# Kernel optimization log

Hardware: AMD Instinct MI355X
Metric: run time of the kernel (lower is better)

## Reference

```python
import jax, jax.numpy as jnp
import numpy as np

N = 12000       # num nodes
E = 384000      # num edges (avg degree 32)
F_IN = 512      # num_feats
H = 64          # gnn_hid_dim (== anchor_dim)
C = 7           # num_cls
SIGMA = 1.0


def setup_inputs() -> dict:
    key = jax.random.key(0)
    ks = jax.random.split(key, 9)
    scale = lambda fan_in: 1.0 / np.sqrt(fan_in)
    return {
        "x": jax.random.normal(ks[0], (N, F_IN), dtype=jnp.float32),
        "W1": jax.random.normal(ks[1], (F_IN, H), dtype=jnp.float32) * scale(F_IN),
        "b1": jnp.zeros((H,), dtype=jnp.float32),
        "W2": jax.random.normal(ks[2], (H, H), dtype=jnp.float32) * scale(H),
        "b2": jnp.zeros((H,), dtype=jnp.float32),
        "aux": jax.random.normal(ks[3], (H,), dtype=jnp.float32),
        "clf_W": jax.random.normal(ks[4], (2 * H, C), dtype=jnp.float32) * scale(2 * H),
        "clf_b": jnp.zeros((C,), dtype=jnp.float32),
        "edge_index": jax.random.randint(ks[5], (2, E), 0, N, dtype=jnp.int64),
    }


def gcn_conv(x, W, b, src, dst, n):
    # GCNConv: D^{-1/2} (A + I) D^{-1/2} X W + b, with self-loops
    h = x @ W                                                   # [N, out]
    deg = jax.ops.segment_sum(jnp.ones(src.shape[0], h.dtype), dst,
                              num_segments=n) + 1.0             # +1 for self-loop
    inv_sqrt = jax.lax.rsqrt(deg)
    norm = inv_sqrt[src] * inv_sqrt[dst]                        # [E]
    agg = jax.ops.segment_sum(h[src] * norm[:, None], dst, num_segments=n)
    agg = agg + h / deg[:, None]                                # self-loop term (norm = 1/deg)
    return agg + b


def reference(x, W1, b1, W2, b2, aux, clf_W, clf_b, edge_index):
    src, dst = edge_index[0], edge_index[1]
    n = x.shape[0]
    h = jax.nn.relu(gcn_conv(x, W1, b1, src, dst, n))
    h = gcn_conv(h, W2, b2, src, dst, n)                        # [N, H]
    # kernel aggregate: pairwise Gaussian kernel on cosine scores
    a = aux / jnp.maximum(jnp.linalg.norm(aux), 1e-12)          # F.normalize
    hn = jnp.maximum(jnp.linalg.norm(h, axis=-1), 1e-8)         # cosine_similarity eps
    score = (h @ a) / hn                                        # [N]
    diff = score[None, :] - score[:, None]                      # [N, N]
    kappa = jnp.exp(-(diff * diff) / (SIGMA * SIGMA))           # [N, N]
    z = (kappa @ h) / jnp.sum(kappa, axis=1, keepdims=True)     # [N, H]
    return jnp.concatenate([h, z], axis=-1) @ clf_W + clf_b     # [N, C]
```

## Files before the change

### kernel.cpp

```cpp
#include <hip/hip_runtime.h>
#include <hip/hip_bf16.h>

#define N_NODES 12000
#define N_EDGES 384000
#define F_IN 512
#define H 64
#define C_CLS 7
#define KTERMS 16
#define PAD 96
#define CSTR 32
#define MOM_BLKS 768
#define MSTR 1040
#define NB 4
#define GEMM_BLKS 375
#define FILL_BLKS 256
#define XS_STR 68

__device__ __forceinline__ float wred_f(float x) {
    #pragma unroll
    for (int o = 32; o > 0; o >>= 1) x += __shfl_xor(x, o);
    return x;
}

__global__ __launch_bounds__(256) void init_k(int* __restrict__ cur,
                                              double* __restrict__ M8) {
    int i = blockIdx.x * 256 + threadIdx.x;
    if (i < N_NODES) cur[i * CSTR] = 0;
    if (i < 8 * MSTR) M8[i] = 0.0;
}

__global__ __launch_bounds__(256) void k1_gemm_fill(const float* __restrict__ x,
                                                    const float* __restrict__ W1,
                                                    const int* __restrict__ ei,
                                                    float* __restrict__ hbuf,
                                                    int* __restrict__ cur,
                                                    int* __restrict__ csrc) {
    const int b = blockIdx.x, t = threadIdx.x;
    if (b < GEMM_BLKS) {
        __shared__ float xs[32 * XS_STR];
        __shared__ float wsm[64 * 64];
        const int tx = t & 15, ty = t >> 4;
        const int i0 = b * 32;
        float acc[2][4] = {};
        for (int k0 = 0; k0 < F_IN; k0 += 64) {
            #pragma unroll
            for (int q = 0; q < 2; ++q) {
                int idx = t + q * 256;
                int row = idx >> 4, kg = idx & 15;
                *(float4*)(&xs[row * XS_STR + kg * 4]) =
                    *(const float4*)(x + (size_t)(i0 + row) * F_IN + k0 + kg * 4);
            }
            #pragma unroll
            for (int q = 0; q < 4; ++q) {
                int idx = t + q * 256;
                int r = idx >> 4, cg = idx & 15;
                *(float4*)(&wsm[r * 64 + cg * 4]) =
                    *(const float4*)(W1 + (size_t)(k0 + r) * H + cg * 4);
            }
            __syncthreads();
            #pragma unroll
            for (int kk0 = 0; kk0 < 64; kk0 += 4) {
                float4 a0 = *(const float4*)(&xs[(ty * 2 + 0) * XS_STR + kk0]);
                float4 a1 = *(const float4*)(&xs[(ty * 2 + 1) * XS_STR + kk0]);
                float4 b0 = *(const float4*)(&wsm[(kk0 + 0) * 64 + tx * 4]);
                float4 b1v = *(const float4*)(&wsm[(kk0 + 1) * 64 + tx * 4]);
                float4 b2v = *(const float4*)(&wsm[(kk0 + 2) * 64 + tx * 4]);
                float4 b3v = *(const float4*)(&wsm[(kk0 + 3) * 64 + tx * 4]);
                acc[0][0] += a0.x * b0.x;  acc[0][1] += a0.x * b0.y;  acc[0][2] += a0.x * b0.z;  acc[0][3] += a0.x * b0.w;
                acc[0][0] += a0.y * b1v.x; acc[0][1] += a0.y * b1v.y; acc[0][2] += a0.y * b1v.z; acc[0][3] += a0.y * b1v.w;
                acc[0][0] += a0.z * b2v.x; acc[0][1] += a0.z * b2v.y; acc[0][2] += a0.z * b2v.z; acc[0][3] += a0.z * b2v.w;
                acc[0][0] += a0.w * b3v.x; acc[0][1] += a0.w * b3v.y; acc[0][2] += a0.w * b3v.z; acc[0][3] += a0.w * b3v.w;
                acc[1][0] += a1.x * b0.x;  acc[1][1] += a1.x * b0.y;  acc[1][2] += a1.x * b0.z;  acc[1][3] += a1.x * b0.w;
                acc[1][0] += a1.y * b1v.x; acc[1][1] += a1.y * b1v.y; acc[1][2] += a1.y * b1v.z; acc[1][3] += a1.y * b1v.w;
                acc[1][0] += a1.z * b2v.x; acc[1][1] += a1.z * b2v.y; acc[1][2] += a1.z * b2v.z; acc[1][3] += a1.z * b2v.w;
                acc[1][0] += a1.w * b3v.x; acc[1][1] += a1.w * b3v.y; acc[1][2] += a1.w * b3v.z; acc[1][3] += a1.w * b3v.w;
            }
            __syncthreads();
        }
        #pragma unroll
        for (int r = 0; r < 2; ++r) {
            int row = i0 + ty * 2 + r;
            *(float4*)(hbuf + (size_t)row * H + tx * 4) =
                make_float4(acc[r][0], acc[r][1], acc[r][2], acc[r][3]);
        }
    } else {
        for (int e = (b - GEMM_BLKS) * 256 + t; e < N_EDGES; e += FILL_BLKS * 256) {
            int s = ei[e];
            int d = ei[N_EDGES + e];
            int pos = atomicAdd(&cur[d * CSTR], 1);
            if (pos < PAD) csrc[d * PAD + pos] = s;
        }
    }
}

__global__ __launch_bounds__(256) void agg1_k(const float* __restrict__ hbuf,
                                              const float* __restrict__ b1,
                                              const int* __restrict__ cur,
                                              const int* __restrict__ csrc,
                                              float* __restrict__ h1) {
    __shared__ int2 sPair[NB * PAD];
    __shared__ int sDeg[NB];
    __shared__ float sIsd[NB];
    const int t = threadIdx.x, f = t & 63, w = t >> 6;
    const int base = blockIdx.x * NB;
    if (t < NB) {
        int d = cur[(base + t) * CSTR];
        sDeg[t] = min(d, PAD);
        sIsd[t] = rsqrtf((float)d + 1.f);
    }
    __syncthreads();
    for (int idx = t; idx < NB * PAD; idx += 256) {
        int n = idx / PAD, e = idx - n * PAD;
        if (e < sDeg[n]) {
            int s = csrc[(base + n) * PAD + e];
            sPair[idx] = make_int2(s, __float_as_int(rsqrtf((float)cur[s * CSTR] + 1.f)));
        }
    }
    __syncthreads();
    const int i = base + w;
    const int deg = sDeg[w];
    const float isd = sIsd[w];
    const int2* pp = sPair + w * PAD;
    float acc = 0.f;
    int e = 0;
    for (; e + 8 <= deg; e += 8) {
        int2 p0 = pp[e], p1 = pp[e+1], p2 = pp[e+2], p3 = pp[e+3];
        int2 p4 = pp[e+4], p5 = pp[e+5], p6 = pp[e+6], p7 = pp[e+7];
        acc += hbuf[p0.x * H + f] * __int_as_float(p0.y)
             + hbuf[p1.x * H + f] * __int_as_float(p1.y)
             + hbuf[p2.x * H + f] * __int_as_float(p2.y)
             + hbuf[p3.x * H + f] * __int_as_float(p3.y)
             + hbuf[p4.x * H + f] * __int_as_float(p4.y)
             + hbuf[p5.x * H + f] * __int_as_float(p5.y)
             + hbuf[p6.x * H + f] * __int_as_float(p6.y)
             + hbuf[p7.x * H + f] * __int_as_float(p7.y);
    }
    for (; e + 4 <= deg; e += 4) {
        int2 p0 = pp[e], p1 = pp[e+1], p2 = pp[e+2], p3 = pp[e+3];
        acc += hbuf[p0.x * H + f] * __int_as_float(p0.y)
             + hbuf[p1.x * H + f] * __int_as_float(p1.y)
             + hbuf[p2.x * H + f] * __int_as_float(p2.y)
             + hbuf[p3.x * H + f] * __int_as_float(p3.y);
    }
    for (; e < deg; ++e) {
        int2 p = pp[e];
        acc += hbuf[p.x * H + f] * __int_as_float(p.y);
    }
    float res = (acc + hbuf[i * H + f] * isd) * isd + b1[f];
    h1[i * H + f] = fmaxf(res, 0.f);
}

__global__ __launch_bounds__(256) void agg2_k(const float* __restrict__ h1,
                                              const float* __restrict__ W2,
                                              const float* __restrict__ b2,
                                              const float* __restrict__ aux,
                                              const int* __restrict__ cur,
                                              const int* __restrict__ csrc,
                                              float* __restrict__ h2,
                                              float* __restrict__ score) {
    __shared__ float w2s[64 * 64];
    __shared__ int2 sPair[NB * PAD];
    __shared__ int sDeg[NB];
    __shared__ float sIsd[NB];
    __shared__ float anorm[64];
    __shared__ float gsh[NB * 64];
    const int t = threadIdx.x, f = t & 63, w = t >> 6;
    const int base = blockIdx.x * NB;
    #pragma unroll
    for (int q = 0; q < 4; ++q) {
        int idx = t + q * 256;
        int r = idx >> 4, c4 = idx & 15;
        *(float4*)(&w2s[r * 64 + c4 * 4]) = *(const float4*)(W2 + r * H + c4 * 4);
    }
    if (t < NB) {
        int d = cur[(base + t) * CSTR];
        sDeg[t] = min(d, PAD);
        sIsd[t] = rsqrtf((float)d + 1.f);
    }
    if (t < 64) {
        float av = aux[t];
        anorm[t] = av * rsqrtf(fmaxf(wred_f(av * av), 1e-24f));
    }
    __syncthreads();
    for (int idx = t; idx < NB * PAD; idx += 256) {
        int n = idx / PAD, e = idx - n * PAD;
        if (e < sDeg[n]) {
            int s = csrc[(base + n) * PAD + e];
            sPair[idx] = make_int2(s, __float_as_int(rsqrtf((float)cur[s * CSTR] + 1.f)));
        }
    }
    __syncthreads();
    const int i = base + w;
    const int deg = sDeg[w];
    const float isd = sIsd[w];
    const int2* pp = sPair + w * PAD;
    float acc = 0.f;
    int e = 0;
    for (; e + 8 <= deg; e += 8) {
        int2 p0 = pp[e], p1 = pp[e+1], p2 = pp[e+2], p3 = pp[e+3];
        int2 p4 = pp[e+4], p5 = pp[e+5], p6 = pp[e+6], p7 = pp[e+7];
        acc += h1[p0.x * H + f] * __int_as_float(p0.y)
             + h1[p1.x * H + f] * __int_as_float(p1.y)
             + h1[p2.x * H + f] * __int_as_float(p2.y)
             + h1[p3.x * H + f] * __int_as_float(p3.y)
             + h1[p4.x * H + f] * __int_as_float(p4.y)
             + h1[p5.x * H + f] * __int_as_float(p5.y)
             + h1[p6.x * H + f] * __int_as_float(p6.y)
             + h1[p7.x * H + f] * __int_as_float(p7.y);
    }
    for (; e + 4 <= deg; e += 4) {
        int2 p0 = pp[e], p1 = pp[e+1], p2 = pp[e+2], p3 = pp[e+3];
        acc += h1[p0.x * H + f] * __int_as_float(p0.y)
             + h1[p1.x * H + f] * __int_as_float(p1.y)
             + h1[p2.x * H + f] * __int_as_float(p2.y)
             + h1[p3.x * H + f] * __int_as_float(p3.y);
    }
    for (; e < deg; ++e) {
        int2 p = pp[e];
        acc += h1[p.x * H + f] * __int_as_float(p.y);
    }
    float g = (acc + h1[i * H + f] * isd) * isd;
    gsh[w * 64 + f] = g;
    __builtin_amdgcn_wave_barrier();
    float hv = b2[f];
    #pragma unroll 16
    for (int k = 0; k < 64; ++k) hv += gsh[w * 64 + k] * w2s[k * 64 + f];
    h2[i * H + f] = hv;
    float dp = wred_f(hv * anorm[f]);
    float nn = wred_f(hv * hv);
    if (f == 0) score[i] = dp / fmaxf(sqrtf(nn), 1e-8f);
}

__global__ __launch_bounds__(256) void momden_k(const float* __restrict__ h2,
                                                const float* __restrict__ score,
                                                double* __restrict__ M8) {
    const int t = threadIdx.x, f = t & 63, g = t >> 6;
    float accM[KTERMS], accD[KTERMS];
    #pragma unroll
    for (int k = 0; k < KTERMS; ++k) { accM[k] = 0.f; accD[k] = 0.f; }
    for (int j = blockIdx.x * 4 + g; j < N_NODES; j += MOM_BLKS * 4) {
        float sj = score[j];
        float wj = expf(-sj * sj);
        float hv = h2[j * H + f];
        float tm = wj * hv, td = wj;
        #pragma unroll
        for (int k = 0; k < KTERMS; ++k) {
            accM[k] += tm; tm *= sj;
            accD[k] += td; td *= sj;
        }
    }
    __shared__ float Msh[4 * KTERMS * 64];
    __shared__ float Dsh[4 * KTERMS];
    #pragma unroll
    for (int k = 0; k < KTERMS; ++k) Msh[(g * KTERMS + k) * 64 + f] = accM[k];
    if (f == 0) {
        #pragma unroll
        for (int k = 0; k < KTERMS; ++k) Dsh[g * KTERMS + k] = accD[k];
    }
    __syncthreads();
    double* Mc = M8 + (size_t)(blockIdx.x & 7) * MSTR;
    for (int idx = t; idx < KTERMS * 64; idx += 256) {
        int k = idx >> 6, ff = idx & 63;
        float sum = Msh[(0 * KTERMS + k) * 64 + ff] + Msh[(1 * KTERMS + k) * 64 + ff]
                  + Msh[(2 * KTERMS + k) * 64 + ff] + Msh[(3 * KTERMS + k) * 64 + ff];
        unsafeAtomicAdd(&Mc[idx], (double)sum);
    }
    if (t < KTERMS) {
        float sum = Dsh[t] + Dsh[KTERMS + t] + Dsh[2 * KTERMS + t] + Dsh[3 * KTERMS + t];
        unsafeAtomicAdd(&Mc[1024 + t], (double)sum);
    }
}

__global__ __launch_bounds__(256) void final_k(const float* __restrict__ h2,
                                               const float* __restrict__ score,
                                               const double* __restrict__ M8,
                                               const float* __restrict__ clfW,
                                               const float* __restrict__ clfb,
                                               float* __restrict__ out) {
    __shared__ float Ms[KTERMS * 64];
    __shared__ float m0s[KTERMS];
    __shared__ float cw[128 * C_CLS];
    __shared__ float cb[8];
    __shared__ float zh[4 * 128];
    const int t = threadIdx.x, f = t & 63, w = t >> 6;
    for (int idx = t; idx < KTERMS * 64; idx += 256) {
        double s = 0.0;
        #pragma unroll
        for (int c = 0; c < 8; ++c) s += M8[(size_t)c * MSTR + idx];
        Ms[idx] = (float)s;
    }
    if (t < KTERMS) {
        double s = 0.0;
        #pragma unroll
        for (int c = 0; c < 8; ++c) s += M8[(size_t)c * MSTR + 1024 + t];
        m0s[t] = (float)s;
    }
    for (int idx = t; idx < 128 * C_CLS; idx += 256) cw[idx] = clfW[idx];
    if (t < C_CLS) cb[t] = clfb[t];
    __syncthreads();
    const int base = blockIdx.x * 16;
    for (int q = 0; q < 4; ++q) {
        int i = base + q * 4 + w;
        float s = score[i];
        float c = expf(-s * s);
        float t2 = 2.f * s;
        float num = 0.f, den = 0.f;
        #pragma unroll
        for (int k = 0; k < KTERMS; ++k) {
            num += c * Ms[k * 64 + f];
            den += c * m0s[k];
            c *= t2 * (1.0f / (float)(k + 1));
        }
        zh[w * 128 + f] = h2[i * H + f];
        zh[w * 128 + 64 + f] = num / den;
        __builtin_amdgcn_wave_barrier();
        if (f < C_CLS) {
            float o = cb[f];
            #pragma unroll 8
            for (int u = 0; u < 128; ++u) o += zh[w * 128 + u] * cw[u * C_CLS + f];
            out[(size_t)i * C_CLS + f] = o;
        }
        __builtin_amdgcn_wave_barrier();
    }
}

extern "C" void kernel_launch(void* const* d_in, const int* in_sizes, int n_in,
                              void* d_out, int out_size, void* d_ws, size_t ws_size,
                              hipStream_t stream) {
    (void)in_sizes; (void)n_in; (void)out_size; (void)ws_size;
    const float* x    = (const float*)d_in[0];
    const float* W1   = (const float*)d_in[1];
    const float* b1   = (const float*)d_in[2];
    const float* W2   = (const float*)d_in[3];
    const float* b2   = (const float*)d_in[4];
    const float* aux  = (const float*)d_in[5];
    const float* clfW = (const float*)d_in[6];
    const float* clfb = (const float*)d_in[7];
    const int*   ei   = (const int*)d_in[8];
    float* out = (float*)d_out;
    char* ws = (char*)d_ws;

    float*  hbuf  = (float*)(ws + 0);
    float*  h1    = (float*)(ws + 3072000);
    float*  h2    = (float*)(ws + 6144000);
    float*  score = (float*)(ws + 9216000);
    int*    csrc  = (int*)  (ws + 9264000);
    int*    cur   = (int*)  (ws + 13872000);
    double* M8    = (double*)(ws + 15408000);

    init_k<<<47, 256, 0, stream>>>(cur, M8);
    k1_gemm_fill<<<GEMM_BLKS + FILL_BLKS, 256, 0, stream>>>(x, W1, ei, hbuf, cur, csrc);
    agg1_k<<<N_NODES / NB, 256, 0, stream>>>(hbuf, b1, cur, csrc, h1);
    agg2_k<<<N_NODES / NB, 256, 0, stream>>>(h1, W2, b2, aux, cur, csrc, h2, score);
    momden_k<<<MOM_BLKS, 256, 0, stream>>>(h2, score, M8);
    final_k<<<750, 256, 0, stream>>>(h2, score, M8, clfW, clfb, out);
}
```

Measured before the change: 95.13 us.

## Split-K the first GEMM with 64-row tiles and atomic accumulation

The X@W1 GEMM now uses 64-row tiles with a 4x4 per-thread register block, and the K dimension is split in two halves across block pairs. The partial results are combined with float atomic adds into hbuf, which init_k now zeroes. The goal is more register reuse per shared-memory load while keeping about the same block count for parallelism. In exchange it adds a zeroing pass over hbuf, atomic traffic, and non-deterministic summation order.

```diff
diff --git a/kernel.cpp b/kernel.cpp
--- a/kernel.cpp
+++ b/kernel.cpp
@@ -12,7 +12,7 @@
 #define MOM_BLKS 768
 #define MSTR 1040
 #define NB 4
-#define GEMM_BLKS 375
+#define GEMM_BLKS 376
 #define FILL_BLKS 256
 #define XS_STR 68
 
@@ -22,11 +22,14 @@
     return x;
 }
 
-__global__ __launch_bounds__(256) void init_k(int* __restrict__ cur,
+__global__ __launch_bounds__(256) void init_k(float* __restrict__ hbuf,
+                                              int* __restrict__ cur,
                                               double* __restrict__ M8) {
-    int i = blockIdx.x * 256 + threadIdx.x;
-    if (i < N_NODES) cur[i * CSTR] = 0;
-    if (i < 8 * MSTR) M8[i] = 0.0;
+    const int tid = blockIdx.x * 256 + threadIdx.x;
+    const float4 z4 = make_float4(0.f, 0.f, 0.f, 0.f);
+    for (int i = tid; i < N_NODES * H / 4; i += 48128) ((float4*)hbuf)[i] = z4;
+    if (tid < N_NODES) cur[tid * CSTR] = 0;
+    if (tid < 8 * MSTR) M8[tid] = 0.0;
 }
 
 __global__ __launch_bounds__(256) void k1_gemm_fill(const float* __restrict__ x,
@@ -37,18 +40,20 @@
                                                     int* __restrict__ csrc) {
     const int b = blockIdx.x, t = threadIdx.x;
     if (b < GEMM_BLKS) {
-        __shared__ float xs[32 * XS_STR];
+        __shared__ float xs[64 * XS_STR];
         __shared__ float wsm[64 * 64];
         const int tx = t & 15, ty = t >> 4;
-        const int i0 = b * 32;
-        float acc[2][4] = {};
-        for (int k0 = 0; k0 < F_IN; k0 += 64) {
+        const int ks = b & 1;
+        const int i0 = (b >> 1) * 64;
+        float acc[4][4] = {};
+        for (int k0 = ks * 256; k0 < ks * 256 + 256; k0 += 64) {
             #pragma unroll
-            for (int q = 0; q < 2; ++q) {
+            for (int q = 0; q < 4; ++q) {
                 int idx = t + q * 256;
                 int row = idx >> 4, kg = idx & 15;
+                int rg = min(i0 + row, N_NODES - 1);
                 *(float4*)(&xs[row * XS_STR + kg * 4]) =
-                    *(const float4*)(x + (size_t)(i0 + row) * F_IN + k0 + kg * 4);
+                    *(const float4*)(x + (size_t)rg * F_IN + k0 + kg * 4);
             }
             #pragma unroll
             for (int q = 0; q < 4; ++q) {
@@ -60,8 +65,10 @@
             __syncthreads();
             #pragma unroll
             for (int kk0 = 0; kk0 < 64; kk0 += 4) {
-                float4 a0 = *(const float4*)(&xs[(ty * 2 + 0) * XS_STR + kk0]);
-                float4 a1 = *(const float4*)(&xs[(ty * 2 + 1) * XS_STR + kk0]);
+                float4 a0 = *(const float4*)(&xs[(ty * 4 + 0) * XS_STR + kk0]);
+                float4 a1 = *(const float4*)(&xs[(ty * 4 + 1) * XS_STR + kk0]);
+                float4 a2 = *(const float4*)(&xs[(ty * 4 + 2) * XS_STR + kk0]);
+                float4 a3 = *(const float4*)(&xs[(ty * 4 + 3) * XS_STR + kk0]);
                 float4 b0 = *(const float4*)(&wsm[(kk0 + 0) * 64 + tx * 4]);
                 float4 b1v = *(const float4*)(&wsm[(kk0 + 1) * 64 + tx * 4]);
                 float4 b2v = *(const float4*)(&wsm[(kk0 + 2) * 64 + tx * 4]);
@@ -74,14 +81,25 @@
                 acc[1][0] += a1.y * b1v.x; acc[1][1] += a1.y * b1v.y; acc[1][2] += a1.y * b1v.z; acc[1][3] += a1.y * b1v.w;
                 acc[1][0] += a1.z * b2v.x; acc[1][1] += a1.z * b2v.y; acc[1][2] += a1.z * b2v.z; acc[1][3] += a1.z * b2v.w;
                 acc[1][0] += a1.w * b3v.x; acc[1][1] += a1.w * b3v.y; acc[1][2] += a1.w * b3v.z; acc[1][3] += a1.w * b3v.w;
+                acc[2][0] += a2.x * b0.x;  acc[2][1] += a2.x * b0.y;  acc[2][2] += a2.x * b0.z;  acc[2][3] += a2.x * b0.w;
+                acc[2][0] += a2.y * b1v.x; acc[2][1] += a2.y * b1v.y; acc[2][2] += a2.y * b1v.z; acc[2][3] += a2.y * b1v.w;
+                acc[2][0] += a2.z * b2v.x; acc[2][1] += a2.z * b2v.y; acc[2][2] += a2.z * b2v.z; acc[2][3] += a2.z * b2v.w;
+                acc[2][0] += a2.w * b3v.x; acc[2][1] += a2.w * b3v.y; acc[2][2] += a2.w * b3v.z; acc[2][3] += a2.w * b3v.w;
+                acc[3][0] += a3.x * b0.x;  acc[3][1] += a3.x * b0.y;  acc[3][2] += a3.x * b0.z;  acc[3][3] += a3.x * b0.w;
+                acc[3][0] += a3.y * b1v.x; acc[3][1] += a3.y * b1v.y; acc[3][2] += a3.y * b1v.z; acc[3][3] += a3.y * b1v.w;
+                acc[3][0] += a3.z * b2v.x; acc[3][1] += a3.z * b2v.y; acc[3][2] += a3.z * b2v.z; acc[3][3] += a3.z * b2v.w;
+                acc[3][0] += a3.w * b3v.x; acc[3][1] += a3.w * b3v.y; acc[3][2] += a3.w * b3v.z; acc[3][3] += a3.w * b3v.w;
             }
             __syncthreads();
         }
         #pragma unroll
-        for (int r = 0; r < 2; ++r) {
-            int row = i0 + ty * 2 + r;
-            *(float4*)(hbuf + (size_t)row * H + tx * 4) =
-                make_float4(acc[r][0], acc[r][1], acc[r][2], acc[r][3]);
+        for (int r = 0; r < 4; ++r) {
+            int row = i0 + ty * 4 + r;
+            if (row < N_NODES) {
+                #pragma unroll
+                for (int j = 0; j < 4; ++j)
+                    unsafeAtomicAdd(&hbuf[(size_t)row * H + tx * 4 + j], acc[r][j]);
+            }
         }
     } else {
         for (int e = (b - GEMM_BLKS) * 256 + t; e < N_EDGES; e += FILL_BLKS * 256) {
@@ -348,7 +366,7 @@
     int*    cur   = (int*)  (ws + 13872000);
     double* M8    = (double*)(ws + 15408000);
 
-    init_k<<<47, 256, 0, stream>>>(cur, M8);
+    init_k<<<188, 256, 0, stream>>>(hbuf, cur, M8);
     k1_gemm_fill<<<GEMM_BLKS + FILL_BLKS, 256, 0, stream>>>(x, W1, ei, hbuf, cur, csrc);
     agg1_k<<<N_NODES / NB, 256, 0, stream>>>(hbuf, b1, cur, csrc, h1);
     agg2_k<<<N_NODES / NB, 256, 0, stream>>>(h1, W2, b2, aux, cur, csrc, h2, score);
```

Result: slower. 109.3 us (+14.9%).

## Use split-bf16 MFMA for the first-layer X·W1 GEMM

Applied to the files above, without the earlier changes.

Replaces the scalar FP32 FMA tiling of x@W1 with MFMA 16x16x32 bf16 instructions, using a three-term hi/lo bf16 split to keep accuracy close to FP32. W1 is pre-split and transposed in the init kernel, x is split on the fly from LDS, and tiles grow to 64 rows per block so half as many GEMM blocks run. The aim is to move the dominant GEMM from vector ALUs to matrix cores. The trade-off is extra conversion work, three MFMAs per product, and slightly lower precision than true FP32.

```diff
diff --git a/kernel.cpp b/kernel.cpp
--- a/kernel.cpp
+++ b/kernel.cpp
@@ -12,9 +12,11 @@
 #define MOM_BLKS 768
 #define MSTR 1040
 #define NB 4
-#define GEMM_BLKS 375
+#define GEMM_BLKS 188
 #define FILL_BLKS 256
-#define XS_STR 68
+
+typedef __attribute__((ext_vector_type(8))) short bf16x8;
+typedef __attribute__((ext_vector_type(4))) float f32x4;
 
 __device__ __forceinline__ float wred_f(float x) {
     #pragma unroll
@@ -22,66 +24,92 @@
     return x;
 }
 
-__global__ __launch_bounds__(256) void init_k(int* __restrict__ cur,
+__global__ __launch_bounds__(256) void init_k(const float* __restrict__ W1,
+                                              unsigned short* __restrict__ w1Th,
+                                              unsigned short* __restrict__ w1Tl,
+                                              int* __restrict__ cur,
                                               double* __restrict__ M8) {
     int i = blockIdx.x * 256 + threadIdx.x;
+    if (i < 64 * 512) {
+        int n = i >> 9, k = i & 511;
+        float v = W1[k * 64 + n];
+        unsigned xb = __float_as_uint(v);
+        float hf = __uint_as_float(xb & 0xffff0000u);
+        w1Th[i] = (unsigned short)(xb >> 16);
+        w1Tl[i] = (unsigned short)(__float_as_uint(v - hf) >> 16);
+    }
     if (i < N_NODES) cur[i * CSTR] = 0;
     if (i < 8 * MSTR) M8[i] = 0.0;
 }
 
 __global__ __launch_bounds__(256) void k1_gemm_fill(const float* __restrict__ x,
-                                                    const float* __restrict__ W1,
+                                                    const unsigned short* __restrict__ w1Th,
+                                                    const unsigned short* __restrict__ w1Tl,
                                                     const int* __restrict__ ei,
                                                     float* __restrict__ hbuf,
                                                     int* __restrict__ cur,
                                                     int* __restrict__ csrc) {
     const int b = blockIdx.x, t = threadIdx.x;
     if (b < GEMM_BLKS) {
-        __shared__ float xs[32 * XS_STR];
-        __shared__ float wsm[64 * 64];
-        const int tx = t & 15, ty = t >> 4;
-        const int i0 = b * 32;
-        float acc[2][4] = {};
-        for (int k0 = 0; k0 < F_IN; k0 += 64) {
+        __shared__ float xs[64 * 68];
+        __shared__ unsigned short wh[64 * 72];
+        __shared__ unsigned short wl[64 * 72];
+        const int l = t & 63, w = t >> 6;
+        const int lm = l & 15, lk = l >> 4;
+        const int i0 = b * 64;
+        f32x4 acc[4];
+        #pragma unroll
+        for (int c = 0; c < 4; ++c) acc[c] = (f32x4){0.f, 0.f, 0.f, 0.f};
+        for (int kc = 0; kc < 8; ++kc) {
+            #pragma unroll
+            for (int q = 0; q < 4; ++q) {
+                int idx = t + q * 256;
+                int row = idx >> 4, kg = idx & 15;
+                int rg = min(i0 + row, N_NODES - 1);
+                *(float4*)(&xs[row * 68 + kg * 4]) =
+                    *(const float4*)(x + (size_t)rg * F_IN + kc * 64 + kg * 4);
+            }
             #pragma unroll
             for (int q = 0; q < 2; ++q) {
                 int idx = t + q * 256;
-                int row = idx >> 4, kg = idx & 15;
-                *(float4*)(&xs[row * XS_STR + kg * 4]) =
-                    *(const float4*)(x + (size_t)(i0 + row) * F_IN + k0 + kg * 4);
-            }
-            #pragma unroll
-            for (int q = 0; q < 4; ++q) {
-                int idx = t + q * 256;
-                int r = idx >> 4, cg = idx & 15;
-                *(float4*)(&wsm[r * 64 + cg * 4]) =
-                    *(const float4*)(W1 + (size_t)(k0 + r) * H + cg * 4);
+                int n = idx >> 3, kg = idx & 7;
+                *(uint4*)(&wh[n * 72 + kg * 8]) =
+                    *(const uint4*)(w1Th + n * 512 + kc * 64 + kg * 8);
+                *(uint4*)(&wl[n * 72 + kg * 8]) =
+                    *(const uint4*)(w1Tl + n * 512 + kc * 64 + kg * 8);
             }
             __syncthreads();
             #pragma unroll
-            for (int kk0 = 0; kk0 < 64; kk0 += 4) {
-                float4 a0 = *(const float4*)(&xs[(ty * 2 + 0) * XS_STR + kk0]);
-                float4 a1 = *(const float4*)(&xs[(ty * 2 + 1) * XS_STR + kk0]);
-                float4 b0 = *(const float4*)(&wsm[(kk0 + 0) * 64 + tx * 4]);
-                float4 b1v = *(const float4*)(&wsm[(kk0 + 1) * 64 + tx * 4]);
-                float4 b2v = *(const float4*)(&wsm[(kk0 + 2) * 64 + tx * 4]);
-                float4 b3v = *(const float4*)(&wsm[(kk0 + 3) * 64 + tx * 4]);
-                acc[0][0] += a0.x * b0.x;  acc[0][1] += a0.x * b0.y;  acc[0][2] += a0.x * b0.z;  acc[0][3] += a0.x * b0.w;
-                acc[0][0] += a0.y * b1v.x; acc[0][1] += a0.y * b1v.y; acc[0][2] += a0.y * b1v.z; acc[0][3] += a0.y * b1v.w;
-                acc[0][0] += a0.z * b2v.x; acc[0][1] += a0.z * b2v.y; acc[0][2] += a0.z * b2v.z; acc[0][3] += a0.z * b2v.w;
-                acc[0][0] += a0.w * b3v.x; acc[0][1] += a0.w * b3v.y; acc[0][2] += a0.w * b3v.z; acc[0][3] += a0.w * b3v.w;
-                acc[1][0] += a1.x * b0.x;  acc[1][1] += a1.x * b0.y;  acc[1][2] += a1.x * b0.z;  acc[1][3] += a1.x * b0.w;
-                acc[1][0] += a1.y * b1v.x; acc[1][1] += a1.y * b1v.y; acc[1][2] += a1.y * b1v.z; acc[1][3] += a1.y * b1v.w;
-                acc[1][0] += a1.z * b2v.x; acc[1][1] += a1.z * b2v.y; acc[1][2] += a1.z * b2v.z; acc[1][3] += a1.z * b2v.w;
-                acc[1][0] += a1.w * b3v.x; acc[1][1] += a1.w * b3v.y; acc[1][2] += a1.w * b3v.z; acc[1][3] += a1.w * b3v.w;
+            for (int ks = 0; ks < 2; ++ks) {
+                const float* ap = &xs[(w * 16 + lm) * 68 + ks * 32 + lk * 8];
+                bf16x8 ah, al;
+                #pragma unroll
+                for (int j = 0; j < 8; ++j) {
+                    float xv = ap[j];
+                    unsigned xb = __float_as_uint(xv);
+                    float hf = __uint_as_float(xb & 0xffff0000u);
+                    ah[j] = (short)(xb >> 16);
+                    al[j] = (short)(__float_as_uint(xv - hf) >> 16);
+                }
+                #pragma unroll
+                for (int c = 0; c < 4; ++c) {
+                    bf16x8 bh = *(const bf16x8*)(&wh[(c * 16 + lm) * 72 + ks * 32 + lk * 8]);
+                    bf16x8 bl = *(const bf16x8*)(&wl[(c * 16 + lm) * 72 + ks * 32 + lk * 8]);
+                    acc[c] = __builtin_amdgcn_mfma_f32_16x16x32_bf16(ah, bh, acc[c], 0, 0, 0);
+                    acc[c] = __builtin_amdgcn_mfma_f32_16x16x32_bf16(ah, bl, acc[c], 0, 0, 0);
+                    acc[c] = __builtin_amdgcn_mfma_f32_16x16x32_bf16(al, bh, acc[c], 0, 0, 0);
+                }
             }
             __syncthreads();
         }
         #pragma unroll
-        for (int r = 0; r < 2; ++r) {
-            int row = i0 + ty * 2 + r;
-            *(float4*)(hbuf + (size_t)row * H + tx * 4) =
-                make_float4(acc[r][0], acc[r][1], acc[r][2], acc[r][3]);
+        for (int c = 0; c < 4; ++c) {
+            #pragma unroll
+            for (int r = 0; r < 4; ++r) {
+                int row = i0 + w * 16 + lk * 4 + r;
+                if (row < N_NODES)
+                    hbuf[(size_t)row * H + c * 16 + lm] = acc[c][r];
+            }
         }
     } else {
         for (int e = (b - GEMM_BLKS) * 256 + t; e < N_EDGES; e += FILL_BLKS * 256) {
@@ -347,9 +375,12 @@
     int*    csrc  = (int*)  (ws + 9264000);
     int*    cur   = (int*)  (ws + 13872000);
     double* M8    = (double*)(ws + 15408000);
-
-    init_k<<<47, 256, 0, stream>>>(cur, M8);
-    k1_gemm_fill<<<GEMM_BLKS + FILL_BLKS, 256, 0, stream>>>(x, W1, ei, hbuf, cur, csrc);
+    unsigned short* w1Th = (unsigned short*)(ws + 15474560);
+    unsigned short* w1Tl = (unsigned short*)(ws + 15540096);
+
+    init_k<<<128, 256, 0, stream>>>(W1, w1Th, w1Tl, cur, M8);
+    k1_gemm_fill<<<GEMM_BLKS + FILL_BLKS, 256, 0, stream>>>(x, w1Th, w1Tl, ei,
+                                                            hbuf, cur, csrc);
     agg1_k<<<N_NODES / NB, 256, 0, stream>>>(hbuf, b1, cur, csrc, h1);
     agg2_k<<<N_NODES / NB, 256, 0, stream>>>(h1, W2, b2, aux, cur, csrc, h2, score);
     momden_k<<<MOM_BLKS, 256, 0, stream>>>(h2, score, M8);
```

Result: slower. 106.2 us (+11.6%).

## Fuse moment accumulation into agg2 and precompute per-edge normalization weights

Applied to the files above, without the earlier changes.

Removes the separate momden kernel by having each agg2 block compute its nodes' Taylor moment terms and atomically add them into 16 double stripes. A new wedge kernel precomputes per-edge rsqrt(deg) once, so both aggregation kernels skip the dependent gather of cur[s]. final_k now handles 48 nodes per block with fewer blocks. The cost is 3000 blocks issuing double atomics instead of 768, which may raise contention, plus an extra kernel launch and an extra buffer read.

```diff
diff --git a/kernel.cpp b/kernel.cpp
--- a/kernel.cpp
+++ b/kernel.cpp
@@ -9,7 +9,7 @@
 #define KTERMS 16
 #define PAD 96
 #define CSTR 32
-#define MOM_BLKS 768
+#define NSTRIPE 16
 #define MSTR 1040
 #define NB 4
 #define GEMM_BLKS 375
@@ -23,10 +23,10 @@
 }
 
 __global__ __launch_bounds__(256) void init_k(int* __restrict__ cur,
-                                              double* __restrict__ M8) {
+                                              double* __restrict__ M16) {
     int i = blockIdx.x * 256 + threadIdx.x;
     if (i < N_NODES) cur[i * CSTR] = 0;
-    if (i < 8 * MSTR) M8[i] = 0.0;
+    for (int j = i; j < NSTRIPE * MSTR; j += 12032) M16[j] = 0.0;
 }
 
 __global__ __launch_bounds__(256) void k1_gemm_fill(const float* __restrict__ x,
@@ -93,10 +93,23 @@
     }
 }
 
+__global__ __launch_bounds__(256) void wedge_k(const int* __restrict__ cur,
+                                               const int* __restrict__ csrc,
+                                               float* __restrict__ wedge) {
+    int idx = blockIdx.x * 256 + threadIdx.x;
+    int n = idx / PAD, e = idx - n * PAD;
+    int deg = min(cur[n * CSTR], PAD);
+    if (e < deg) {
+        int s = csrc[idx];
+        wedge[idx] = rsqrtf((float)cur[s * CSTR] + 1.f);
+    }
+}
+
 __global__ __launch_bounds__(256) void agg1_k(const float* __restrict__ hbuf,
                                               const float* __restrict__ b1,
                                               const int* __restrict__ cur,
                                               const int* __restrict__ csrc,
+                                              const float* __restrict__ wedge,
                                               float* __restrict__ h1) {
     __shared__ int2 sPair[NB * PAD];
     __shared__ int sDeg[NB];
@@ -112,8 +125,8 @@
     for (int idx = t; idx < NB * PAD; idx += 256) {
         int n = idx / PAD, e = idx - n * PAD;
         if (e < sDeg[n]) {
-            int s = csrc[(base + n) * PAD + e];
-            sPair[idx] = make_int2(s, __float_as_int(rsqrtf((float)cur[s * CSTR] + 1.f)));
+            int g = base * PAD + idx;
+            sPair[idx] = make_int2(csrc[g], __float_as_int(wedge[g]));
         }
     }
     __syncthreads();
@@ -150,20 +163,24 @@
     h1[i * H + f] = fmaxf(res, 0.f);
 }
 
-__global__ __launch_bounds__(256) void agg2_k(const float* __restrict__ h1,
-                                              const float* __restrict__ W2,
-                                              const float* __restrict__ b2,
-                                              const float* __restrict__ aux,
-                                              const int* __restrict__ cur,
-                                              const int* __restrict__ csrc,
-                                              float* __restrict__ h2,
-                                              float* __restrict__ score) {
+__global__ __launch_bounds__(256) void agg2m_k(const float* __restrict__ h1,
+                                               const float* __restrict__ W2,
+                                               const float* __restrict__ b2,
+                                               const float* __restrict__ aux,
+                                               const int* __restrict__ cur,
+                                               const int* __restrict__ csrc,
+                                               const float* __restrict__ wedge,
+                                               float* __restrict__ h2,
+                                               float* __restrict__ score,
+                                               double* __restrict__ M16) {
     __shared__ float w2s[64 * 64];
     __shared__ int2 sPair[NB * PAD];
     __shared__ int sDeg[NB];
     __shared__ float sIsd[NB];
     __shared__ float anorm[64];
     __shared__ float gsh[NB * 64];
+    __shared__ float Msh[NB * KTERMS * 64];
+    __shared__ float Dsh[NB * KTERMS];
     const int t = threadIdx.x, f = t & 63, w = t >> 6;
     const int base = blockIdx.x * NB;
     #pragma unroll
@@ -185,8 +202,8 @@
     for (int idx = t; idx < NB * PAD; idx += 256) {
         int n = idx / PAD, e = idx - n * PAD;
         if (e < sDeg[n]) {
-            int s = csrc[(base + n) * PAD + e];
-            sPair[idx] = make_int2(s, __float_as_int(rsqrtf((float)cur[s * CSTR] + 1.f)));
+            int g = base * PAD + idx;
+            sPair[idx] = make_int2(csrc[g], __float_as_int(wedge[g]));
         }
     }
     __syncthreads();
@@ -228,37 +245,20 @@
     h2[i * H + f] = hv;
     float dp = wred_f(hv * anorm[f]);
     float nn = wred_f(hv * hv);
-    if (f == 0) score[i] = dp / fmaxf(sqrtf(nn), 1e-8f);
-}
-
-__global__ __launch_bounds__(256) void momden_k(const float* __restrict__ h2,
-                                                const float* __restrict__ score,
-                                                double* __restrict__ M8) {
-    const int t = threadIdx.x, f = t & 63, g = t >> 6;
-    float accM[KTERMS], accD[KTERMS];
+    float sc = dp / fmaxf(sqrtf(nn), 1e-8f);
+    sc = __shfl(sc, 0);
+    if (f == 0) score[i] = sc;
+    float wj = expf(-sc * sc);
+    float tm = wj * hv;
     #pragma unroll
-    for (int k = 0; k < KTERMS; ++k) { accM[k] = 0.f; accD[k] = 0.f; }
-    for (int j = blockIdx.x * 4 + g; j < N_NODES; j += MOM_BLKS * 4) {
-        float sj = score[j];
-        float wj = expf(-sj * sj);
-        float hv = h2[j * H + f];
-        float tm = wj * hv, td = wj;
-        #pragma unroll
-        for (int k = 0; k < KTERMS; ++k) {
-            accM[k] += tm; tm *= sj;
-            accD[k] += td; td *= sj;
-        }
-    }
-    __shared__ float Msh[4 * KTERMS * 64];
-    __shared__ float Dsh[4 * KTERMS];
-    #pragma unroll
-    for (int k = 0; k < KTERMS; ++k) Msh[(g * KTERMS + k) * 64 + f] = accM[k];
+    for (int k = 0; k < KTERMS; ++k) { Msh[(w * KTERMS + k) * 64 + f] = tm; tm *= sc; }
     if (f == 0) {
-        #pragma unroll
-        for (int k = 0; k < KTERMS; ++k) Dsh[g * KTERMS + k] = accD[k];
-    }
-    __syncthreads();
-    double* Mc = M8 + (size_t)(blockIdx.x & 7) * MSTR;
+        float td = wj;
+        #pragma unroll
+        for (int k = 0; k < KTERMS; ++k) { Dsh[w * KTERMS + k] = td; td *= sc; }
+    }
+    __syncthreads();
+    double* Mc = M16 + (size_t)(blockIdx.x & (NSTRIPE - 1)) * MSTR;
     for (int idx = t; idx < KTERMS * 64; idx += 256) {
         int k = idx >> 6, ff = idx & 63;
         float sum = Msh[(0 * KTERMS + k) * 64 + ff] + Msh[(1 * KTERMS + k) * 64 + ff]
@@ -273,7 +273,7 @@
 
 __global__ __launch_bounds__(256) void final_k(const float* __restrict__ h2,
                                                const float* __restrict__ score,
-                                               const double* __restrict__ M8,
+                                               const double* __restrict__ M16,
                                                const float* __restrict__ clfW,
                                                const float* __restrict__ clfb,
                                                float* __restrict__ out) {
@@ -286,20 +286,20 @@
     for (int idx = t; idx < KTERMS * 64; idx += 256) {
         double s = 0.0;
         #pragma unroll
-        for (int c = 0; c < 8; ++c) s += M8[(size_t)c * MSTR + idx];
+        for (int c = 0; c < NSTRIPE; ++c) s += M16[(size_t)c * MSTR + idx];
         Ms[idx] = (float)s;
     }
     if (t < KTERMS) {
         double s = 0.0;
         #pragma unroll
-        for (int c = 0; c < 8; ++c) s += M8[(size_t)c * MSTR + 1024 + t];
+        for (int c = 0; c < NSTRIPE; ++c) s += M16[(size_t)c * MSTR + 1024 + t];
         m0s[t] = (float)s;
     }
     for (int idx = t; idx < 128 * C_CLS; idx += 256) cw[idx] = clfW[idx];
     if (t < C_CLS) cb[t] = clfb[t];
     __syncthreads();
-    const int base = blockIdx.x * 16;
-    for (int q = 0; q < 4; ++q) {
+    const int base = blockIdx.x * 48;
+    for (int q = 0; q < 12; ++q) {
         int i = base + q * 4 + w;
         float s = score[i];
         float c = expf(-s * s);
@@ -345,13 +345,15 @@
     float*  h2    = (float*)(ws + 6144000);
     float*  score = (float*)(ws + 9216000);
     int*    csrc  = (int*)  (ws + 9264000);
-    int*    cur   = (int*)  (ws + 13872000);
-    double* M8    = (double*)(ws + 15408000);
-
-    init_k<<<47, 256, 0, stream>>>(cur, M8);
+    float*  wedge = (float*)(ws + 13872000);
+    int*    cur   = (int*)  (ws + 18480000);
+    double* M16   = (double*)(ws + 20016000);
+
+    init_k<<<47, 256, 0, stream>>>(cur, M16);
     k1_gemm_fill<<<GEMM_BLKS + FILL_BLKS, 256, 0, stream>>>(x, W1, ei, hbuf, cur, csrc);
-    agg1_k<<<N_NODES / NB, 256, 0, stream>>>(hbuf, b1, cur, csrc, h1);
-    agg2_k<<<N_NODES / NB, 256, 0, stream>>>(h1, W2, b2, aux, cur, csrc, h2, score);
-    momden_k<<<MOM_BLKS, 256, 0, stream>>>(h2, score, M8);
-    final_k<<<750, 256, 0, stream>>>(h2, score, M8, clfW, clfb, out);
-}
+    wedge_k<<<4500, 256, 0, stream>>>(cur, csrc, wedge);
+    agg1_k<<<N_NODES / NB, 256, 0, stream>>>(hbuf, b1, cur, csrc, wedge, h1);
+    agg2m_k<<<N_NODES / NB, 256, 0, stream>>>(h1, W2, b2, aux, cur, csrc, wedge,
+                                              h2, score, M16);
+    final_k<<<250, 256, 0, stream>>>(h2, score, M16, clfW, clfb, out);
+}
```

After: 113.2 us. +19.0%, slower.
